# Performance work log

Measured on AMD Instinct MI355X. Metric: run time of the kernel, lower is better.

The kernel has to match this reference:

```python
import jax, jax.numpy as jnp
import numpy as np

B, S, PAST = 4, 2048, 2048
D_IN, D_H, D_FF = 2048, 2048, 8192


def setup_inputs() -> dict:
    key = jax.random.key(0)
    ks = jax.random.split(key, 13)
    s = lambda k, shape, fan: jax.random.normal(k, shape, jnp.float32) * (fan ** -0.5)
    return {
        "x": jax.random.normal(ks[0], (B, S, D_IN), jnp.float32),
        "k_cache": jax.random.normal(ks[1], (B, PAST, D_H), jnp.float32),
        "v_cache": jax.random.normal(ks[2], (B, PAST, D_H), jnp.float32),
        "Wq": s(ks[3], (D_IN, D_H), D_IN), "bq": jnp.zeros((D_H,), jnp.float32),
        "Wk": s(ks[4], (D_IN, D_H), D_IN), "bk": jnp.zeros((D_H,), jnp.float32),
        "Wv": s(ks[5], (D_IN, D_H), D_IN), "bv": jnp.zeros((D_H,), jnp.float32),
        "Wff": s(ks[6], (D_H, D_FF), D_H), "bff": jnp.zeros((D_FF,), jnp.float32),
        "Wout": s(ks[7], (D_FF, D_H), D_FF), "bout": jnp.zeros((D_H,), jnp.float32),
    }


def reference(x, k_cache, v_cache, Wq, bq, Wk, bk, Wv, bv, Wff, bff, Wout, bout):
    # Projections: [B,S,D_H]
    q = x @ Wq + bq
    k_new = x @ Wk + bk
    v_new = x @ Wv + bv
    # KV-cache append along sequence dim
    k = jnp.concatenate([k_cache, k_new], axis=1)  # [B, PAST+S, D_H]
    v = jnp.concatenate([v_cache, v_new], axis=1)
    # Scores [B, S, PAST+S]; original uses Softmax(dim=1) -> over QUERY axis
    scores = jnp.einsum("bqd,bkd->bqk", q, k)
    attn = jax.nn.softmax(scores, axis=1)
    ctx = jnp.einsum("bqk,bkd->bqd", attn, v)  # [B, S, D_H]
    # FFN (no nonlinearity in original)
    out = (ctx @ Wff + bff) @ Wout + bout  # [B, S, D_H]
    return out, (k, v)
```

## Files before the change

kernel.cpp:

```cpp
#include <hip/hip_runtime.h>

typedef _Float16 f16;
typedef _Float16 f16x8 __attribute__((ext_vector_type(8)));
typedef _Float16 f16x4 __attribute__((ext_vector_type(4)));
typedef float    f32x4 __attribute__((ext_vector_type(4)));

#define GLOAD_LDS16(g, s) __builtin_amdgcn_global_load_lds( \
    (__attribute__((address_space(1))) void*)(g),           \
    (__attribute__((address_space(3))) void*)(s), 16, 0, 0)

__global__ __launch_bounds__(512, 2) void gemm_nt256(
    const f16* __restrict__ A, int lda, long long Abat,
    const f16* __restrict__ B, int ldb, long long Bbat,
    float* Cf, int ldcf, long long Cfbat,
    f16* Ch, int ldch, long long Chbat,
    const float* __restrict__ bias,
    int K, int rdiv, int rskip, int radd)
{
    extern __shared__ f16 smem[];
    f16* As = smem;
    f16* Bs = smem + 32768;

    const int bz = blockIdx.z;
    A += (long long)bz * Abat;
    B += (long long)bz * Bbat;
    if (Cf) Cf += (long long)bz * Cfbat;
    if (Ch) Ch += (long long)bz * Chbat;

    const int tid = threadIdx.x;
    const int l = tid & 63, w = tid >> 6;

    const int nbx = gridDim.x;
    const int nwg = nbx * gridDim.y;
    const int lin = blockIdx.y * nbx + blockIdx.x;
    const int id = (lin & 7) * (nwg >> 3) + (lin >> 3);
    const int tile_n = (id % nbx) << 8;
    const int tile_m = (id / nbx) << 8;

    const int wm = (w >> 2) << 7;
    const int wn = (w & 3) << 6;

    const f16* Ag = A + (long long)tile_m * lda;
    const f16* Bg = B + (long long)tile_n * ldb;

    const int lr16 = l & 15, lhi = l >> 4, llo8 = l & 7, lrr = l >> 3;
    const f16* aStage = Ag + (long long)(w * 8 + lrr) * lda + ((llo8 ^ lrr) << 3);
    const f16* bStage = Bg + (long long)(w * 8 + lrr) * ldb + ((llo8 ^ lrr) << 3);
    const int stLds = w * 512;

    f32x4 acc[8][4] = {};

    auto stage = [&](int dst, int k0) {
        const f16* ag = aStage + k0;
        const f16* bg = bStage + k0;
        f16* ad = As + dst * 16384 + stLds;
        f16* bd = Bs + dst * 16384 + stLds;
        #pragma unroll
        for (int j = 0; j < 4; ++j) {
            GLOAD_LDS16(ag + (long long)j * 64 * lda, ad + j * 4096);
            GLOAD_LDS16(bg + (long long)j * 64 * ldb, bd + j * 4096);
        }
    };

    const int NT = K >> 6;

    stage(0, 0);
    asm volatile("s_waitcnt vmcnt(0)" ::: "memory");
    __builtin_amdgcn_s_barrier();

    for (int kt = 0; kt < NT; ++kt) {
        const int cur = kt & 1;
        const f16* Ab = As + cur * 16384;
        const f16* Bb = Bs + cur * 16384;
        f16x8 bf[4][2];
        #pragma unroll
        for (int p = 0; p < 4; ++p) {
            f16x8 af[2][2];
            #pragma unroll
            for (int i = 0; i < 2; ++i) {
                const int row = wm + (2 * p + i) * 16 + lr16;
                #pragma unroll
                for (int kk = 0; kk < 2; ++kk)
                    af[i][kk] = *(const f16x8*)&Ab[row * 64 + (((kk * 4 + lhi) ^ llo8) << 3)];
            }
            if (p == 0) {
                #pragma unroll
                for (int nf = 0; nf < 4; ++nf) {
                    const int row = wn + nf * 16 + lr16;
                    #pragma unroll
                    for (int kk = 0; kk < 2; ++kk)
                        bf[nf][kk] = *(const f16x8*)&Bb[row * 64 + (((kk * 4 + lhi) ^ llo8) << 3)];
                }
                if (kt + 1 < NT) stage(cur ^ 1, (kt + 1) << 6);
            }
            __builtin_amdgcn_s_barrier();
            __builtin_amdgcn_s_setprio(1);
            #pragma unroll
            for (int i = 0; i < 2; ++i)
                #pragma unroll
                for (int nf = 0; nf < 4; ++nf)
                    #pragma unroll
                    for (int kk = 0; kk < 2; ++kk)
                        acc[2 * p + i][nf] = __builtin_amdgcn_mfma_f32_16x16x32_f16(
                            af[i][kk], bf[nf][kk], acc[2 * p + i][nf], 0, 0, 0);
            __builtin_amdgcn_s_setprio(0);
            __builtin_amdgcn_s_barrier();
        }
        asm volatile("s_waitcnt vmcnt(0)" ::: "memory");
        __builtin_amdgcn_s_barrier();
    }

    const int lrow4 = lhi << 2, lcol = lr16;
    #pragma unroll
    for (int nf = 0; nf < 4; ++nf) {
        const int gn = tile_n + wn + nf * 16 + lcol;
        const float bb = bias ? bias[gn] : 0.f;
        #pragma unroll
        for (int mf = 0; mf < 8; ++mf) {
            #pragma unroll
            for (int r = 0; r < 4; ++r) {
                const int gm = tile_m + wm + mf * 16 + lrow4 + r;
                const int crow = gm + radd + rskip * (gm / rdiv);
                const float v = acc[mf][nf][r] + bb;
                if (Cf) Cf[(long long)crow * ldcf + gn] = v;
                if (Ch) Ch[(long long)crow * ldch + gn] = (f16)v;
            }
        }
    }
}

__global__ void k_f32_to_f16(const float* __restrict__ in, f16* __restrict__ out, long long n4)
{
    long long i = (long long)blockIdx.x * 256 + threadIdx.x;
    if (i >= n4) return;
    float4 v = ((const float4*)in)[i];
    f16x4 h = { (f16)v.x, (f16)v.y, (f16)v.z, (f16)v.w };
    ((f16x4*)out)[i] = h;
}

__global__ void k_cache_copy(const float* __restrict__ src, float* __restrict__ dstf,
                             f16* __restrict__ dsth)
{
    long long i4 = (long long)blockIdx.x * 256 + threadIdx.x;
    long long i = i4 * 4;
    if (i >= 16777216LL) return;
    int b = (int)(i >> 22);
    long long o = i + ((long long)b << 22);
    float4 v = ((const float4*)src)[i4];
    *(float4*)(dstf + o) = v;
    if (dsth) {
        f16x4 h = { (f16)v.x, (f16)v.y, (f16)v.z, (f16)v.w };
        *(f16x4*)(dsth + o) = h;
    }
}

__global__ void k_transpose_f32_f16(const float* __restrict__ in, f16* __restrict__ out,
                                    int R, int C, long long inbat, long long outbat)
{
    __shared__ float t[64][65];
    in += (long long)blockIdx.z * inbat;
    out += (long long)blockIdx.z * outbat;
    const int r0 = blockIdx.y * 64, c0 = blockIdx.x * 64;
    const int tx = threadIdx.x & 63, ty = threadIdx.x >> 6;
    #pragma unroll
    for (int i = 0; i < 64; i += 4)
        t[ty + i][tx] = in[(long long)(r0 + ty + i) * C + (c0 + tx)];
    __syncthreads();
    #pragma unroll
    for (int i = 0; i < 64; i += 4)
        out[(long long)(c0 + ty + i) * R + (r0 + tx)] = (f16)t[tx][ty + i];
}

__global__ void k_softmax_q(const float* __restrict__ sc, f16* __restrict__ attn)
{
    const long long boff = (long long)blockIdx.z * 2048 * 4096;
    const float* Sb = sc + boff;
    f16* Ab = attn + boff;
    const int lc = threadIdx.x & 31;
    const int qg = threadIdx.x >> 5;
    const int col = blockIdx.x * 32 + lc;

    float m = -3.0e38f, s = 0.f;
    for (int q = qg; q < 2048; q += 8) {
        float x = Sb[(long long)q * 4096 + col];
        if (x > m) { s = s * __expf(m - x) + 1.f; m = x; }
        else         s += __expf(x - m);
    }
    __shared__ float ms[8][32], ss[8][32], Mf[32], If[32];
    ms[qg][lc] = m; ss[qg][lc] = s;
    __syncthreads();
    if (threadIdx.x < 32) {
        float M = ms[0][lc];
        #pragma unroll
        for (int i = 1; i < 8; i++) M = fmaxf(M, ms[i][lc]);
        float tt = 0.f;
        #pragma unroll
        for (int i = 0; i < 8; i++) tt += ss[i][lc] * __expf(ms[i][lc] - M);
        Mf[lc] = M; If[lc] = 1.f / tt;
    }
    __syncthreads();
    const float M = Mf[lc], inv = If[lc];
    for (int q = qg; q < 2048; q += 8) {
        float x = Sb[(long long)q * 4096 + col];
        Ab[(long long)q * 4096 + col] = (f16)(__expf(x - M) * inv);
    }
}

extern "C" void kernel_launch(void* const* d_in, const int* in_sizes, int n_in,
                              void* d_out, int out_size, void* d_ws, size_t ws_size,
                              hipStream_t stream)
{
    const float* x    = (const float*)d_in[0];
    const float* kc   = (const float*)d_in[1];
    const float* vc   = (const float*)d_in[2];
    const float* Wq   = (const float*)d_in[3];
    const float* bq   = (const float*)d_in[4];
    const float* Wk   = (const float*)d_in[5];
    const float* bk   = (const float*)d_in[6];
    const float* Wv   = (const float*)d_in[7];
    const float* bv   = (const float*)d_in[8];
    const float* Wff  = (const float*)d_in[9];
    const float* bff  = (const float*)d_in[10];
    const float* Wout = (const float*)d_in[11];
    const float* bout = (const float*)d_in[12];

    float* out   = (float*)d_out;
    float* out_k = out + 16777216LL;
    float* out_v = out_k + 33554432LL;

    char* p = (char*)d_ws;
    auto alloc = [&](size_t bytes) { char* r = p; p += (bytes + 255) & ~255ULL; return r; };
    f16* xh     = (f16*)alloc(33554432);
    f16* qh     = (f16*)alloc(33554432);
    f16* kh     = (f16*)alloc(67108864);
    f16* vth    = (f16*)alloc(67108864);
    f16* wqt    = (f16*)alloc(8388608);
    f16* wkt    = (f16*)alloc(8388608);
    f16* wvt    = (f16*)alloc(8388608);
    f16* wfft   = (f16*)alloc(33554432);
    f16* woutt  = (f16*)alloc(33554432);
    f16* ctxh   = (f16*)alloc(33554432);
    float* scores = (float*)alloc(134217728);
    f16* hh     = (f16*)scores;
    f16* attnh  = (f16*)xh;
    (void)ws_size; (void)in_sizes; (void)n_in; (void)out_size;

    const int NOREMAP = 1 << 30;
    const int SMEM = 131072;

    static int smem_set = 0;
    if (!smem_set) {
        hipFuncSetAttribute((const void*)gemm_nt256,
                            hipFuncAttributeMaxDynamicSharedMemorySize, SMEM);
        smem_set = 1;
    }

    k_f32_to_f16<<<16384, 256, 0, stream>>>(x, xh, 4194304LL);
    k_transpose_f32_f16<<<dim3(32, 32, 1),  256, 0, stream>>>(Wq,   wqt,   2048, 2048, 0, 0);
    k_transpose_f32_f16<<<dim3(32, 32, 1),  256, 0, stream>>>(Wk,   wkt,   2048, 2048, 0, 0);
    k_transpose_f32_f16<<<dim3(32, 32, 1),  256, 0, stream>>>(Wv,   wvt,   2048, 2048, 0, 0);
    k_transpose_f32_f16<<<dim3(128, 32, 1), 256, 0, stream>>>(Wff,  wfft,  2048, 8192, 0, 0);
    k_transpose_f32_f16<<<dim3(32, 128, 1), 256, 0, stream>>>(Wout, woutt, 8192, 2048, 0, 0);
    k_cache_copy<<<16384, 256, 0, stream>>>(kc, out_k, kh);
    k_cache_copy<<<16384, 256, 0, stream>>>(vc, out_v, nullptr);

    dim3 gproj(8, 32, 1);
    gemm_nt256<<<gproj, 512, SMEM, stream>>>(xh, 2048, 0, wqt, 2048, 0,
        nullptr, 0, 0, qh, 2048, 0, bq, 2048, NOREMAP, 0, 0);
    gemm_nt256<<<gproj, 512, SMEM, stream>>>(xh, 2048, 0, wkt, 2048, 0,
        out_k, 2048, 0, kh, 2048, 0, bk, 2048, 2048, 2048, 2048);
    gemm_nt256<<<gproj, 512, SMEM, stream>>>(xh, 2048, 0, wvt, 2048, 0,
        out_v, 2048, 0, nullptr, 0, 0, bv, 2048, 2048, 2048, 2048);

    k_transpose_f32_f16<<<dim3(32, 64, 4), 256, 0, stream>>>(out_v, vth, 4096, 2048,
                                                             8388608LL, 8388608LL);

    gemm_nt256<<<dim3(16, 8, 4), 512, SMEM, stream>>>(qh, 2048, 4194304LL, kh, 2048, 8388608LL,
        scores, 4096, 8388608LL, nullptr, 0, 0, nullptr, 2048, NOREMAP, 0, 0);

    k_softmax_q<<<dim3(128, 1, 4), 256, 0, stream>>>(scores, attnh);

    gemm_nt256<<<dim3(8, 8, 4), 512, SMEM, stream>>>(attnh, 4096, 8388608LL, vth, 4096, 8388608LL,
        nullptr, 0, 0, ctxh, 2048, 4194304LL, nullptr, 4096, NOREMAP, 0, 0);

    gemm_nt256<<<dim3(32, 32, 1), 512, SMEM, stream>>>(ctxh, 2048, 0, wfft, 2048, 0,
        nullptr, 0, 0, hh, 8192, 0, bff, 2048, NOREMAP, 0, 0);

    gemm_nt256<<<dim3(8, 32, 1), 512, SMEM, stream>>>(hh, 8192, 0, woutt, 8192, 0,
        out, 2048, 0, nullptr, 0, 0, bout, 8192, NOREMAP, 0, 0);
}
```

Baseline: 1.887 ms.

## Switch GEMM mainloop to 4-stage BK=32 pipeline with split A/B staging

Restructures the 256x256 NT GEMM main loop from a double-buffered K=64 tile to a four-slot ring of K=32 tiles, keeping three tiles in flight. A and B loads for future tiles are issued separately in the two halves of each iteration, with vmcnt waits tuned so only the oldest tile must have landed. The LDS swizzle is changed to match the 32-wide rows. This aims to hide global-load latency better, at the cost of more barriers per unit of K and a different bank-conflict pattern.

```diff
diff --git a/kernel.cpp b/kernel.cpp
--- a/kernel.cpp
+++ b/kernel.cpp
@@ -18,8 +18,6 @@
     int K, int rdiv, int rskip, int radd)
 {
     extern __shared__ f16 smem[];
-    f16* As = smem;
-    f16* Bs = smem + 32768;
 
     const int bz = blockIdx.z;
     A += (long long)bz * Abat;
@@ -43,74 +41,84 @@
     const f16* Ag = A + (long long)tile_m * lda;
     const f16* Bg = B + (long long)tile_n * ldb;
 
-    const int lr16 = l & 15, lhi = l >> 4, llo8 = l & 7, lrr = l >> 3;
-    const f16* aStage = Ag + (long long)(w * 8 + lrr) * lda + ((llo8 ^ lrr) << 3);
-    const f16* bStage = Bg + (long long)(w * 8 + lrr) * ldb + ((llo8 ^ lrr) << 3);
-    const int stLds = w * 512;
+    const int lr16 = l & 15;
+    const int cx = (((l >> 4) ^ ((l >> 1) & 3)) << 3);
+
+    const int srow = w * 16 + (l >> 2);
+    const int gchunk = (l & 3) ^ ((l >> 3) & 3);
+    const f16* aStage = Ag + (long long)srow * lda + (gchunk << 3);
+    const f16* bStage = Bg + (long long)srow * ldb + (gchunk << 3);
+    const int stDst = w * 512;
 
     f32x4 acc[8][4] = {};
 
-    auto stage = [&](int dst, int k0) {
-        const f16* ag = aStage + k0;
-        const f16* bg = bStage + k0;
-        f16* ad = As + dst * 16384 + stLds;
-        f16* bd = Bs + dst * 16384 + stLds;
-        #pragma unroll
-        for (int j = 0; j < 4; ++j) {
-            GLOAD_LDS16(ag + (long long)j * 64 * lda, ad + j * 4096);
-            GLOAD_LDS16(bg + (long long)j * 64 * ldb, bd + j * 4096);
-        }
+    auto stageA = [&](int t) {
+        f16* dst = smem + (t & 3) * 16384 + stDst;
+        const f16* src = aStage + t * 32;
+        GLOAD_LDS16(src, dst);
+        GLOAD_LDS16(src + (long long)128 * lda, dst + 4096);
     };
-
-    const int NT = K >> 6;
-
-    stage(0, 0);
-    asm volatile("s_waitcnt vmcnt(0)" ::: "memory");
+    auto stageB = [&](int t) {
+        f16* dst = smem + (t & 3) * 16384 + 8192 + stDst;
+        const f16* src = bStage + t * 32;
+        GLOAD_LDS16(src, dst);
+        GLOAD_LDS16(src + (long long)128 * ldb, dst + 4096);
+    };
+
+    const int NT = K >> 5;
+
+    stageA(0); stageB(0);
+    stageA(1); stageB(1);
+    stageA(2); stageB(2);
+    asm volatile("s_waitcnt vmcnt(8)" ::: "memory");
     __builtin_amdgcn_s_barrier();
 
     for (int kt = 0; kt < NT; ++kt) {
-        const int cur = kt & 1;
-        const f16* Ab = As + cur * 16384;
-        const f16* Bb = Bs + cur * 16384;
-        f16x8 bf[4][2];
-        #pragma unroll
-        for (int p = 0; p < 4; ++p) {
-            f16x8 af[2][2];
+        const f16* Ab = smem + (kt & 3) * 16384;
+        const f16* Bb = Ab + 8192;
+        f16x8 af[4], bf[4];
+
+        #pragma unroll
+        for (int nf = 0; nf < 4; ++nf)
+            bf[nf] = *(const f16x8*)&Bb[(wn + nf * 16 + lr16) * 32 + cx];
+        #pragma unroll
+        for (int mf = 0; mf < 4; ++mf)
+            af[mf] = *(const f16x8*)&Ab[(wm + mf * 16 + lr16) * 32 + cx];
+        if (kt + 3 < NT) stageA(kt + 3);
+        __builtin_amdgcn_s_barrier();
+        __builtin_amdgcn_s_setprio(1);
+        #pragma unroll
+        for (int mf = 0; mf < 4; ++mf)
             #pragma unroll
-            for (int i = 0; i < 2; ++i) {
-                const int row = wm + (2 * p + i) * 16 + lr16;
-                #pragma unroll
-                for (int kk = 0; kk < 2; ++kk)
-                    af[i][kk] = *(const f16x8*)&Ab[row * 64 + (((kk * 4 + lhi) ^ llo8) << 3)];
-            }
-            if (p == 0) {
-                #pragma unroll
-                for (int nf = 0; nf < 4; ++nf) {
-                    const int row = wn + nf * 16 + lr16;
-                    #pragma unroll
-                    for (int kk = 0; kk < 2; ++kk)
-                        bf[nf][kk] = *(const f16x8*)&Bb[row * 64 + (((kk * 4 + lhi) ^ llo8) << 3)];
-                }
-                if (kt + 1 < NT) stage(cur ^ 1, (kt + 1) << 6);
-            }
-            __builtin_amdgcn_s_barrier();
-            __builtin_amdgcn_s_setprio(1);
+            for (int nf = 0; nf < 4; ++nf)
+                acc[mf][nf] = __builtin_amdgcn_mfma_f32_16x16x32_f16(
+                    af[mf], bf[nf], acc[mf][nf], 0, 0, 0);
+        __builtin_amdgcn_s_setprio(0);
+        __builtin_amdgcn_s_barrier();
+
+        #pragma unroll
+        for (int mf = 0; mf < 4; ++mf)
+            af[mf] = *(const f16x8*)&Ab[(wm + (mf + 4) * 16 + lr16) * 32 + cx];
+        if (kt + 3 < NT) stageB(kt + 3);
+        __builtin_amdgcn_s_barrier();
+        __builtin_amdgcn_s_setprio(1);
+        #pragma unroll
+        for (int mf = 0; mf < 4; ++mf)
             #pragma unroll
-            for (int i = 0; i < 2; ++i)
-                #pragma unroll
-                for (int nf = 0; nf < 4; ++nf)
-                    #pragma unroll
-                    for (int kk = 0; kk < 2; ++kk)
-                        acc[2 * p + i][nf] = __builtin_amdgcn_mfma_f32_16x16x32_f16(
-                            af[i][kk], bf[nf][kk], acc[2 * p + i][nf], 0, 0, 0);
-            __builtin_amdgcn_s_setprio(0);
+            for (int nf = 0; nf < 4; ++nf)
+                acc[mf + 4][nf] = __builtin_amdgcn_mfma_f32_16x16x32_f16(
+                    af[mf], bf[nf], acc[mf + 4][nf], 0, 0, 0);
+        __builtin_amdgcn_s_setprio(0);
+
+        if (kt + 1 < NT) {
+            if (kt + 3 < NT)      asm volatile("s_waitcnt vmcnt(8)" ::: "memory");
+            else if (kt + 2 < NT) asm volatile("s_waitcnt vmcnt(4)" ::: "memory");
+            else                  asm volatile("s_waitcnt vmcnt(0)" ::: "memory");
             __builtin_amdgcn_s_barrier();
         }
-        asm volatile("s_waitcnt vmcnt(0)" ::: "memory");
-        __builtin_amdgcn_s_barrier();
-    }
-
-    const int lrow4 = lhi << 2, lcol = lr16;
+    }
+
+    const int lrow4 = (l >> 4) << 2, lcol = lr16;
     #pragma unroll
     for (int nf = 0; nf < 4; ++nf) {
         const int gn = tile_n + wn + nf * 16 + lcol;
```

New measurement: 1.899 ms. No clear change (+0.6%).
